# Kernel tuning notes

Hardware: AMD Instinct MI355X
Metric: run time of the kernel (lower is better)

The kernel has to match this reference:

```python
import jax, jax.numpy as jnp
import numpy as np

B, C, L, E = 2048, 128, 16, 10      # atoms, channels, num_ell=(lmax+1)^2, elements
P3, P2, P1 = 23, 4, 1               # num CG paths per correlation order
U_DENSITY = 0.15                    # CG-like U tensors are highly sparse


def _sparse_u(key, shape):
    k1, k2 = jax.random.split(key)
    vals = jax.random.normal(k1, shape, dtype=jnp.float32)
    mask = jax.random.uniform(k2, shape) < U_DENSITY
    return jnp.where(mask, vals, 0.0)


def setup_inputs() -> dict:
    key = jax.random.key(0)
    ks = jax.random.split(key, 8)
    x = jax.random.normal(ks[0], (B, C, L), dtype=jnp.float32)
    y = jax.random.uniform(ks[1], (B, E), dtype=jnp.float32)  # element attrs
    U3 = _sparse_u(ks[2], (L, L, L, P3))
    U2 = _sparse_u(ks[3], (L, L, P2))
    U1 = _sparse_u(ks[4], (L, P1))
    W3 = jax.random.normal(ks[5], (E, P3, C), dtype=jnp.float32) / P3
    W2 = jax.random.normal(ks[6], (E, P2, C), dtype=jnp.float32) / P2
    W1 = jax.random.normal(ks[7], (E, P1, C), dtype=jnp.float32) / P1
    return {"x": x, "y": y, "U3": U3, "U2": U2, "U1": U1,
            "W3": W3, "W2": W2, "W1": W1}


def reference(x, y, U3, U2, U1, W3, W2, W1):
    # nu=3 main contraction: 'wxik,ekc,bci,be->bcwx'
    out = jnp.einsum('wxik,ekc,bci,be->bcwx', U3, W3, x, y, optimize='optimal')  # [B,C,L,L]
    # nu=2: weighting then feature contraction
    c2 = jnp.einsum('wxk,ekc,be->bcwx', U2, W2, y, optimize='optimal') + out
    out = jnp.einsum('bcwi,bci->bcw', c2, x)                                     # [B,C,L]
    # nu=1
    c1 = jnp.einsum('wk,ekc,be->bcw', U1, W1, y, optimize='optimal') + out
    out = jnp.einsum('bci,bci->bc', c1, x)                                       # [B,C]
    return out.reshape(out.shape[0], -1)
```

## Files before the change

### kernel.cpp

```cpp
#include <hip/hip_runtime.h>
#include <hip/hip_bf16.h>

typedef __attribute__((ext_vector_type(8))) short short8;
typedef __attribute__((ext_vector_type(16))) float f32x16;

#define LL 16
#define NP3 23
#define NE 10
#define NC 128
#define KI 24
#define NSK 24
#define NT 8
#define MB 128
#define THREADS 256

static __device__ __forceinline__ short f2bs(float f) {
    __hip_bfloat16 h = __float2bfloat16(f);
    short s;
    __builtin_memcpy(&s, &h, 2);
    return s;
}

__global__ void build_B(const float* __restrict__ U3, const float* __restrict__ U2,
                        __hip_bfloat16* __restrict__ Bf) {
    int g = blockIdx.x;
    int t = g / NSK, s = g % NSK;
    int lane = threadIdx.x;
    int col  = t * 32 + (lane & 31);
    int hi   = lane >> 5;
    short8 v;
#pragma unroll
    for (int j = 0; j < 8; ++j) {
        int K = s * 16 + hi * 8 + j;
        int i = K / KI, kk = K - i * KI;
        float f;
        if (kk < NP3)    f = U3[((size_t)col * LL + i) * NP3 + kk];
        else if (i < 4)  f = U2[col * 4 + i];
        else             f = 0.f;
        v[j] = f2bs(f);
    }
    *reinterpret_cast<short8*>(Bf + ((size_t)g * 64 + lane) * 8) = v;
}

#define BUILD_A(HIOFF)                                                        \
    _Pragma("unroll")                                                         \
    for (int s = 0; s < NSK; ++s) {                                           \
        short8 av;                                                            \
        _Pragma("unroll")                                                     \
        for (int j = 0; j < 8; ++j) {                                         \
            const int K  = s * 16 + (HIOFF) + j;                              \
            const int i  = K / KI;                                            \
            const int kk = K - i * KI;                                        \
            float f = (kk < NP3) ? xr[i] * wr[kk]                             \
                                 : ((i < 4) ? w2r[i] : 0.f);                  \
            av[j] = f2bs(f);                                                  \
        }                                                                     \
        A[s] = av;                                                            \
    }

__global__ __launch_bounds__(THREADS, 2)
void contract_k(const float* __restrict__ x, const float* __restrict__ y,
                const float* __restrict__ W3, const float* __restrict__ W2,
                const float* __restrict__ W1, const float* __restrict__ U1,
                const __hip_bfloat16* __restrict__ Bf, float* __restrict__ out) {
    __shared__ float xs[MB][17];
    __shared__ float wys[MB][29];

    const int tid = threadIdx.x;
    const int m0  = blockIdx.x * MB;
    const int b   = blockIdx.x;

    for (int idx = tid; idx < MB * LL; idx += THREADS)
        xs[idx >> 4][idx & 15] = x[(size_t)m0 * LL + idx];
    __syncthreads();

    float yv[NE];
#pragma unroll
    for (int e = 0; e < NE; ++e) yv[e] = y[(size_t)b * NE + e];

    for (int u = tid; u < 29 * MB; u += THREADS) {
        int idx = u >> 7, r = u & (MB - 1);
        float s = 0.f;
        if (idx < NP3) {
#pragma unroll
            for (int e = 0; e < NE; ++e) s += yv[e] * W3[(e * NP3 + idx) * NC + r];
        } else if (idx < 27) {
#pragma unroll
            for (int e = 0; e < NE; ++e) s += yv[e] * W2[(e * 4 + (idx - NP3)) * NC + r];
        } else if (idx == 27) {
#pragma unroll
            for (int e = 0; e < NE; ++e) s += yv[e] * W1[e * NC + r];
        } else {
#pragma unroll
            for (int w = 0; w < LL; ++w) s += U1[w] * xs[r][w];
        }
        wys[r][idx] = s;
    }
    __syncthreads();

    const int lane = tid & 63;
    const int wb   = tid >> 6;
    const int l31  = lane & 31;
    const int hi   = lane >> 5;
    const int bsel = l31 >> 4;
    const int arow = wb * 32 + l31;

    short8 A[NSK];
    {
        float xr[LL], wr[NP3], w2r[4];
#pragma unroll
        for (int i = 0; i < LL; ++i) xr[i] = xs[arow][i];
#pragma unroll
        for (int k = 0; k < NP3; ++k) wr[k] = wys[arow][k];
#pragma unroll
        for (int i = 0; i < 4; ++i) w2r[i] = wys[arow][NP3 + i];
        if (hi == 0) { BUILD_A(0) } else { BUILD_A(8) }
    }

    float xx[16];
#pragma unroll
    for (int q = 0; q < 16; ++q) {
        int rowq = (wb << 5) + (q & 3) + ((q >> 2) << 3) + (hi << 2);
        xx[q] = xs[rowq][lane & 15];
    }

    const short8* Bv = reinterpret_cast<const short8*>(Bf);
    short8 bf[6];
#pragma unroll
    for (int j = 0; j < 6; ++j) bf[j] = Bv[(size_t)j * 64 + lane];

    float acc_out[16];
#pragma unroll
    for (int q = 0; q < 16; ++q) acc_out[q] = 0.f;

#pragma unroll
    for (int t = 0; t < NT; ++t) {
        f32x16 acc;
#pragma unroll
        for (int q = 0; q < 16; ++q) acc[q] = 0.f;
#pragma unroll
        for (int s = 0; s < NSK; ++s) {
            const int g = t * NSK + s;
            acc = __builtin_amdgcn_mfma_f32_32x32x16_bf16(A[s], bf[g % 6], acc, 0, 0, 0);
            if (g + 6 < NT * NSK)
                bf[g % 6] = Bv[(size_t)(g + 6) * 64 + lane];
        }
#pragma unroll
        for (int q = 0; q < 16; ++q) {
            int rowq = (wb << 5) + (q & 3) + ((q >> 2) << 3) + (hi << 2);
            float xw = xs[rowq][2 * t + bsel];
            acc_out[q] += acc[q] * xx[q] * xw;
        }
    }

#pragma unroll
    for (int q = 0; q < 16; ++q) {
        float v = acc_out[q];
        v += __shfl_xor(v, 1);
        v += __shfl_xor(v, 2);
        v += __shfl_xor(v, 4);
        v += __shfl_xor(v, 8);
        v += __shfl_xor(v, 16);
        if (l31 == 0) {
            int rowq = (wb << 5) + (q & 3) + ((q >> 2) << 3) + (hi << 2);
            out[m0 + rowq] = v + wys[rowq][27] * wys[rowq][28];
        }
    }
}

extern "C" void kernel_launch(void* const* d_in, const int* in_sizes, int n_in,
                              void* d_out, int out_size, void* d_ws, size_t ws_size,
                              hipStream_t stream) {
    const float* x  = (const float*)d_in[0];
    const float* y  = (const float*)d_in[1];
    const float* U3 = (const float*)d_in[2];
    const float* U2 = (const float*)d_in[3];
    const float* U1 = (const float*)d_in[4];
    const float* W3 = (const float*)d_in[5];
    const float* W2 = (const float*)d_in[6];
    const float* W1 = (const float*)d_in[7];
    __hip_bfloat16* Bf = (__hip_bfloat16*)d_ws;

    build_B<<<NT * NSK, 64, 0, stream>>>(U3, U2, Bf);
    contract_k<<<2048, THREADS, 0, stream>>>(x, y, W3, W2, W1, U1, Bf, (float*)d_out);
}
```

Baseline: 116.0 us.

## Stage B fragments through double-buffered LDS with direct global-to-LDS loads

```diff
diff --git a/kernel.cpp b/kernel.cpp
--- a/kernel.cpp
+++ b/kernel.cpp
@@ -13,6 +13,7 @@
 #define NT 8
 #define MB 128
 #define THREADS 256
+#define TILE_B 24576
 
 static __device__ __forceinline__ short f2bs(float f) {
     __hip_bfloat16 h = __float2bfloat16(f);
@@ -58,17 +59,35 @@
         A[s] = av;                                                            \
     }
 
+static __device__ __forceinline__ void gload_lds16(const void* g, void* l) {
+    __builtin_amdgcn_global_load_lds((const __attribute__((address_space(1))) void*)g,
+                                     (__attribute__((address_space(3))) void*)l, 16, 0, 0);
+}
+
 __global__ __launch_bounds__(THREADS, 2)
 void contract_k(const float* __restrict__ x, const float* __restrict__ y,
                 const float* __restrict__ W3, const float* __restrict__ W2,
                 const float* __restrict__ W1, const float* __restrict__ U1,
                 const __hip_bfloat16* __restrict__ Bf, float* __restrict__ out) {
+    __shared__ __align__(16) char Bs[2][TILE_B];
     __shared__ float xs[MB][17];
     __shared__ float wys[MB][29];
 
     const int tid = threadIdx.x;
     const int m0  = blockIdx.x * MB;
     const int b   = blockIdx.x;
+
+#define STAGE(tile, buf)                                                      \
+    {                                                                         \
+        const char* gsrc = (const char*)Bf + (size_t)(tile) * TILE_B + tid * 16; \
+        char* ldst = &Bs[buf][tid * 16];                                      \
+        _Pragma("unroll")                                                     \
+        for (int j = 0; j < 6; ++j)                                           \
+            gload_lds16(gsrc + j * 4096, ldst + j * 4096);                    \
+    }
+
+    STAGE(0, 0);
+    STAGE(1, 1);
 
     for (int idx = tid; idx < MB * LL; idx += THREADS)
         xs[idx >> 4][idx & 15] = x[(size_t)m0 * LL + idx];
@@ -124,26 +143,20 @@
         xx[q] = xs[rowq][lane & 15];
     }
 
-    const short8* Bv = reinterpret_cast<const short8*>(Bf);
-    short8 bf[6];
-#pragma unroll
-    for (int j = 0; j < 6; ++j) bf[j] = Bv[(size_t)j * 64 + lane];
-
     float acc_out[16];
 #pragma unroll
     for (int q = 0; q < 16; ++q) acc_out[q] = 0.f;
 
 #pragma unroll
     for (int t = 0; t < NT; ++t) {
+        const int cur = t & 1;
         f32x16 acc;
 #pragma unroll
         for (int q = 0; q < 16; ++q) acc[q] = 0.f;
 #pragma unroll
         for (int s = 0; s < NSK; ++s) {
-            const int g = t * NSK + s;
-            acc = __builtin_amdgcn_mfma_f32_32x32x16_bf16(A[s], bf[g % 6], acc, 0, 0, 0);
-            if (g + 6 < NT * NSK)
-                bf[g % 6] = Bv[(size_t)(g + 6) * 64 + lane];
+            short8 bfrag = *reinterpret_cast<const short8*>(&Bs[cur][(s * 64 + lane) * 16]);
+            acc = __builtin_amdgcn_mfma_f32_32x32x16_bf16(A[s], bfrag, acc, 0, 0, 0);
         }
 #pragma unroll
         for (int q = 0; q < 16; ++q) {
@@ -151,6 +164,8 @@
             float xw = xs[rowq][2 * t + bsel];
             acc_out[q] += acc[q] * xx[q] * xw;
         }
+        __syncthreads();
+        if (t + 2 < NT) STAGE(t + 2, cur);
     }
 
 #pragma unroll
@@ -166,6 +181,7 @@
             out[m0 + rowq] = v + wys[rowq][27] * wys[rowq][28];
         }
     }
+#undef STAGE
 }
 
 extern "C" void kernel_launch(void* const* d_in, const int* in_sizes, int n_in,
```

Measured after the change: 202.1 us. 1.74x slower.

## Split K across two blocks, stage B in LDS, share B fragments across row tiles

Applied to the files above, without the earlier changes.

```diff
diff --git a/kernel.cpp b/kernel.cpp
--- a/kernel.cpp
+++ b/kernel.cpp
@@ -3,16 +3,17 @@
 
 typedef __attribute__((ext_vector_type(8))) short short8;
 typedef __attribute__((ext_vector_type(16))) float f32x16;
+typedef __attribute__((ext_vector_type(4))) float f32x4;
 
 #define LL 16
 #define NP3 23
 #define NE 10
 #define NC 128
 #define KI 24
-#define NSK 24
-#define NT 8
+#define NSKH 12
 #define MB 128
-#define THREADS 256
+#define THREADS 512
+#define BHALF 98304
 
 static __device__ __forceinline__ short f2bs(float f) {
     __hip_bfloat16 h = __float2bfloat16(f);
@@ -23,8 +24,10 @@
 
 __global__ void build_B(const float* __restrict__ U3, const float* __restrict__ U2,
                         __hip_bfloat16* __restrict__ Bf) {
-    int g = blockIdx.x;
-    int t = g / NSK, s = g % NSK;
+    int g   = blockIdx.x;
+    int kh  = g / 96, r96 = g % 96;
+    int t   = r96 / NSKH, s12 = r96 % NSKH;
+    int s   = kh * NSKH + s12;
     int lane = threadIdx.x;
     int col  = t * 32 + (lane & 31);
     int hi   = lane >> 5;
@@ -42,20 +45,20 @@
     *reinterpret_cast<short8*>(Bf + ((size_t)g * 64 + lane) * 8) = v;
 }
 
-#define BUILD_A(HIOFF)                                                        \
+#define BUILD_A(DST, KB)                                                      \
     _Pragma("unroll")                                                         \
-    for (int s = 0; s < NSK; ++s) {                                           \
+    for (int s = 0; s < NSKH; ++s) {                                          \
         short8 av;                                                            \
         _Pragma("unroll")                                                     \
         for (int j = 0; j < 8; ++j) {                                         \
-            const int K  = s * 16 + (HIOFF) + j;                              \
+            const int K  = (KB) + s * 16 + j;                                 \
             const int i  = K / KI;                                            \
             const int kk = K - i * KI;                                        \
             float f = (kk < NP3) ? xr[i] * wr[kk]                             \
                                  : ((i < 4) ? w2r[i] : 0.f);                  \
             av[j] = f2bs(f);                                                  \
         }                                                                     \
-        A[s] = av;                                                            \
+        DST[s] = av;                                                          \
     }
 
 __global__ __launch_bounds__(THREADS, 2)
@@ -63,12 +66,23 @@
                 const float* __restrict__ W3, const float* __restrict__ W2,
                 const float* __restrict__ W1, const float* __restrict__ U1,
                 const __hip_bfloat16* __restrict__ Bf, float* __restrict__ out) {
-    __shared__ float xs[MB][17];
-    __shared__ float wys[MB][29];
-
-    const int tid = threadIdx.x;
-    const int m0  = blockIdx.x * MB;
-    const int b   = blockIdx.x;
+    __shared__ __align__(16) char Bs[BHALF];
+    __shared__ float xs[MB][20];
+    __shared__ float wys[MB][36];
+    __shared__ float part[MB][4];
+
+    const int tid    = threadIdx.x;
+    const int rowblk = blockIdx.x >> 1;
+    const int kh     = blockIdx.x & 1;
+    const int m0     = rowblk * MB;
+    const int b      = rowblk;
+
+    f32x4 st[12];
+    {
+        const f32x4* p = reinterpret_cast<const f32x4*>(Bf) + (size_t)kh * (BHALF / 16) + tid;
+#pragma unroll
+        for (int j = 0; j < 12; ++j) st[j] = p[j * THREADS];
+    }
 
     for (int idx = tid; idx < MB * LL; idx += THREADS)
         xs[idx >> 4][idx & 15] = x[(size_t)m0 * LL + idx];
@@ -96,17 +110,26 @@
         }
         wys[r][idx] = s;
     }
+
+    {
+        f32x4* q = reinterpret_cast<f32x4*>(Bs) + tid;
+#pragma unroll
+        for (int j = 0; j < 12; ++j) q[j * THREADS] = st[j];
+    }
     __syncthreads();
 
     const int lane = tid & 63;
-    const int wb   = tid >> 6;
+    const int wv   = tid >> 6;
+    const int rp   = wv & 1;
+    const int nh   = wv >> 1;
     const int l31  = lane & 31;
     const int hi   = lane >> 5;
     const int bsel = l31 >> 4;
-    const int arow = wb * 32 + l31;
-
-    short8 A[NSK];
-    {
+
+    short8 A2[2][NSKH];
+#pragma unroll
+    for (int rr = 0; rr < 2; ++rr) {
+        const int arow = (rp * 2 + rr) * 32 + l31;
         float xr[LL], wr[NP3], w2r[4];
 #pragma unroll
         for (int i = 0; i < LL; ++i) xr[i] = xs[arow][i];
@@ -114,57 +137,73 @@
         for (int k = 0; k < NP3; ++k) wr[k] = wys[arow][k];
 #pragma unroll
         for (int i = 0; i < 4; ++i) w2r[i] = wys[arow][NP3 + i];
-        if (hi == 0) { BUILD_A(0) } else { BUILD_A(8) }
-    }
-
-    float xx[16];
-#pragma unroll
-    for (int q = 0; q < 16; ++q) {
-        int rowq = (wb << 5) + (q & 3) + ((q >> 2) << 3) + (hi << 2);
-        xx[q] = xs[rowq][lane & 15];
-    }
-
-    const short8* Bv = reinterpret_cast<const short8*>(Bf);
-    short8 bf[6];
-#pragma unroll
-    for (int j = 0; j < 6; ++j) bf[j] = Bv[(size_t)j * 64 + lane];
-
-    float acc_out[16];
-#pragma unroll
-    for (int q = 0; q < 16; ++q) acc_out[q] = 0.f;
-
-#pragma unroll
-    for (int t = 0; t < NT; ++t) {
-        f32x16 acc;
-#pragma unroll
-        for (int q = 0; q < 16; ++q) acc[q] = 0.f;
-#pragma unroll
-        for (int s = 0; s < NSK; ++s) {
-            const int g = t * NSK + s;
-            acc = __builtin_amdgcn_mfma_f32_32x32x16_bf16(A[s], bf[g % 6], acc, 0, 0, 0);
-            if (g + 6 < NT * NSK)
-                bf[g % 6] = Bv[(size_t)(g + 6) * 64 + lane];
-        }
+        if (kh == 0) {
+            if (hi == 0) { BUILD_A(A2[rr], 0) }   else { BUILD_A(A2[rr], 8) }
+        } else {
+            if (hi == 0) { BUILD_A(A2[rr], 192) } else { BUILD_A(A2[rr], 200) }
+        }
+    }
+
+    float xx[2][16];
+#pragma unroll
+    for (int rr = 0; rr < 2; ++rr)
 #pragma unroll
         for (int q = 0; q < 16; ++q) {
-            int rowq = (wb << 5) + (q & 3) + ((q >> 2) << 3) + (hi << 2);
-            float xw = xs[rowq][2 * t + bsel];
-            acc_out[q] += acc[q] * xx[q] * xw;
-        }
-    }
-
-#pragma unroll
-    for (int q = 0; q < 16; ++q) {
-        float v = acc_out[q];
-        v += __shfl_xor(v, 1);
-        v += __shfl_xor(v, 2);
-        v += __shfl_xor(v, 4);
-        v += __shfl_xor(v, 8);
-        v += __shfl_xor(v, 16);
-        if (l31 == 0) {
-            int rowq = (wb << 5) + (q & 3) + ((q >> 2) << 3) + (hi << 2);
-            out[m0 + rowq] = v + wys[rowq][27] * wys[rowq][28];
-        }
+            int rowq = ((rp * 2 + rr) << 5) + (q & 3) + ((q >> 2) << 3) + (hi << 2);
+            xx[rr][q] = xs[rowq][lane & 15];
+        }
+
+    float acc_out[2][16];
+#pragma unroll
+    for (int rr = 0; rr < 2; ++rr)
+#pragma unroll
+        for (int q = 0; q < 16; ++q) acc_out[rr][q] = 0.f;
+
+    const short8* BsV = reinterpret_cast<const short8*>(Bs);
+#pragma unroll
+    for (int tt = 0; tt < 2; ++tt) {
+        const int t = nh * 2 + tt;
+        f32x16 a0, a1;
+#pragma unroll
+        for (int q = 0; q < 16; ++q) { a0[q] = 0.f; a1[q] = 0.f; }
+        __builtin_amdgcn_s_setprio(1);
+#pragma unroll
+        for (int s = 0; s < NSKH; ++s) {
+            short8 bfrag = BsV[(t * NSKH + s) * 64 + lane];
+            a0 = __builtin_amdgcn_mfma_f32_32x32x16_bf16(A2[0][s], bfrag, a0, 0, 0, 0);
+            a1 = __builtin_amdgcn_mfma_f32_32x32x16_bf16(A2[1][s], bfrag, a1, 0, 0, 0);
+        }
+        __builtin_amdgcn_s_setprio(0);
+#pragma unroll
+        for (int q = 0; q < 16; ++q) {
+            int r0 = ((rp * 2 + 0) << 5) + (q & 3) + ((q >> 2) << 3) + (hi << 2);
+            int r1 = ((rp * 2 + 1) << 5) + (q & 3) + ((q >> 2) << 3) + (hi << 2);
+            acc_out[0][q] += a0[q] * xx[0][q] * xs[r0][2 * t + bsel];
+            acc_out[1][q] += a1[q] * xx[1][q] * xs[r1][2 * t + bsel];
+        }
+    }
+
+#pragma unroll
+    for (int rr = 0; rr < 2; ++rr)
+#pragma unroll
+        for (int q = 0; q < 16; ++q) {
+            float v = acc_out[rr][q];
+            v += __shfl_xor(v, 1);
+            v += __shfl_xor(v, 2);
+            v += __shfl_xor(v, 4);
+            v += __shfl_xor(v, 8);
+            v += __shfl_xor(v, 16);
+            if (l31 == 0) {
+                int rowq = ((rp * 2 + rr) << 5) + (q & 3) + ((q >> 2) << 3) + (hi << 2);
+                part[rowq][nh] = v;
+            }
+        }
+    __syncthreads();
+
+    if (tid < MB) {
+        float v = part[tid][0] + part[tid][1] + part[tid][2] + part[tid][3];
+        if (kh == 0) v += wys[tid][27] * wys[tid][28];
+        atomicAdd(out + m0 + tid, v);
     }
 }
 
@@ -181,6 +220,7 @@
     const float* W1 = (const float*)d_in[7];
     __hip_bfloat16* Bf = (__hip_bfloat16*)d_ws;
 
-    build_B<<<NT * NSK, 64, 0, stream>>>(U3, U2, Bf);
-    contract_k<<<2048, THREADS, 0, stream>>>(x, y, W3, W2, W1, U1, Bf, (float*)d_out);
-}
+    hipMemsetAsync(d_out, 0, (size_t)out_size * sizeof(float), stream);
+    build_B<<<192, 64, 0, stream>>>(U3, U2, Bf);
+    contract_k<<<4096, THREADS, 0, stream>>>(x, y, W3, W2, W1, U1, Bf, (float*)d_out);
+}
```

New measurement: 259.6 us. +123.8%, slower.
